# Performance work log

Hardware: AMD Instinct MI355X
Metric: run time of the kernel (lower is better)

## Reference

```python
import jax, jax.numpy as jnp
import numpy as np

# Model constants (from TinyRecursiveModel defaults)
IN = 200        # input feature dim (hard-coded Linear(200, d_model))
D = 64          # d_model
NH = 2          # nhead (head_dim = 32); with seq_len=1 attention is trivial
FF = 64         # dim_feedforward
LAYERS = 2      # TransformerEncoder num_layers
STEPS = 16      # recursion_steps
B = 65536       # batch size
EPS = 1e-5      # torch LayerNorm eps


def setup_inputs() -> dict:
    key = jax.random.key(0)
    ks = jax.random.split(key, 14)
    w = lambda k, shape, s=0.05: (jax.random.normal(k, shape, jnp.float32) * s)
    return {
        "x": jax.random.normal(ks[0], (B, IN), jnp.float32),
        # input_proj: Linear(200, 64)
        "input_w": w(ks[1], (D, IN)), "input_b": w(ks[2], (D,)),
        # per-layer MHA: packed in_proj (q,k,v) and out_proj, stacked over LAYERS
        "Wqkv": w(ks[3], (LAYERS, 3 * D, D)), "bqkv": w(ks[4], (LAYERS, 3 * D)),
        "Wo": w(ks[5], (LAYERS, D, D)), "bo": w(ks[6], (LAYERS, D)),
        "ln1_g": jnp.ones((LAYERS, D), jnp.float32), "ln1_b": jnp.zeros((LAYERS, D), jnp.float32),
        # per-layer FFN: Linear(64,64) -> relu -> Linear(64,64)
        "W1": w(ks[7], (LAYERS, FF, D)), "b1": w(ks[8], (LAYERS, FF)),
        "W2": w(ks[9], (LAYERS, D, FF)), "b2": w(ks[10], (LAYERS, D)),
        "ln2_g": jnp.ones((LAYERS, D), jnp.float32), "ln2_b": jnp.zeros((LAYERS, D), jnp.float32),
        # output_proj: Linear(64, 1)
        "out_w": w(ks[11], (1, D)), "out_b": w(ks[12], (1,)),
    }


def _ln(x, g, b):
    m = jnp.mean(x, axis=-1, keepdims=True)
    v = jnp.var(x, axis=-1, keepdims=True)
    return (x - m) * jax.lax.rsqrt(v + EPS) * g + b


def reference(x, input_w, input_b, Wqkv, bqkv, Wo, bo, ln1_g, ln1_b,
              W1, b1, W2, b2, ln2_g, ln2_b, out_w, out_b):
    h = x @ input_w.T + input_b  # [B, D]; seq dim of size 1 is kept implicit

    def layer(h, l):
        # seq_len == 1: softmax over a single key is identically 1, so the
        # attention output equals V exactly (Q/K have zero influence & zero grad).
        Wv = Wqkv[l, 2 * D:3 * D]
        bv = bqkv[l, 2 * D:3 * D]
        v = h @ Wv.T + bv                     # [B, D]
        sa = v @ Wo[l].T + bo[l]              # out_proj
        h = _ln(h + sa, ln1_g[l], ln1_b[l])   # post-norm (torch default)
        ff = jax.nn.relu(h @ W1[l].T + b1[l]) @ W2[l].T + b2[l]
        return _ln(h + ff, ln2_g[l], ln2_b[l])

    def step(h, _):
        for l in range(LAYERS):  # 2 structurally distinct layers
            h = layer(h, l)
        return h, None

    h, _ = jax.lax.scan(step, h, None, length=STEPS)
    out = h @ out_w.T + out_b  # [B, 1]
    return out[:, 0]           # squeeze -> [B]
```

## Files before the change

kernel.cpp:

```cpp
#include <hip/hip_runtime.h>


using f16x8 = __attribute__((ext_vector_type(8))) _Float16;
using f32x4 = __attribute__((ext_vector_type(4))) float;

#define DI __device__ __forceinline__

namespace {

constexpr int RS = 144;
constexpr float EPS = 1e-5f;

DI unsigned packh2(float a, float b) {
  _Float16 lo = (_Float16)a, hi = (_Float16)b;
  unsigned short ul = __builtin_bit_cast(unsigned short, lo);
  unsigned short uh = __builtin_bit_cast(unsigned short, hi);
  return ((unsigned)uh << 16) | (unsigned)ul;
}

DI f16x8 cvt8h(f32x4 a, f32x4 b) {
  f16x8 r;
  r[0] = (_Float16)a[0]; r[1] = (_Float16)a[1];
  r[2] = (_Float16)a[2]; r[3] = (_Float16)a[3];
  r[4] = (_Float16)b[0]; r[5] = (_Float16)b[1];
  r[6] = (_Float16)b[2]; r[7] = (_Float16)b[3];
  return r;
}

DI unsigned pkmax0(unsigned t) {
  unsigned r;
  asm("v_pk_max_f16 %0, %1, 0" : "=v"(r) : "v"(t));
  return r;
}

DI void swap16(unsigned& a, unsigned& b) {
#if __has_builtin(__builtin_amdgcn_permlane16_swap)
  auto r = __builtin_amdgcn_permlane16_swap(a, b, false, false);
  a = r[0]; b = r[1];
#else
  unsigned ax = (unsigned)__shfl_xor((int)a, 16);
  unsigned bx = (unsigned)__shfl_xor((int)b, 16);
  bool odd = (threadIdx.x & 16) != 0;
  unsigned na = odd ? bx : a;
  unsigned nb = odd ? b : ax;
  a = na; b = nb;
#endif
}
DI void swap32(unsigned& a, unsigned& b) {
#if __has_builtin(__builtin_amdgcn_permlane32_swap)
  auto r = __builtin_amdgcn_permlane32_swap(a, b, false, false);
  a = r[0]; b = r[1];
#else
  unsigned ax = (unsigned)__shfl_xor((int)a, 32);
  unsigned bx = (unsigned)__shfl_xor((int)b, 32);
  bool hi = (threadIdx.x & 32) != 0;
  unsigned na = hi ? bx : a;
  unsigned nb = hi ? b : ax;
  a = na; b = nb;
#endif
}

DI float reduce4(float x) {
  unsigned a = __builtin_bit_cast(unsigned, x), b = a;
  swap16(a, b);
  float x1 = __builtin_bit_cast(float, a) + __builtin_bit_cast(float, b);
  unsigned c = __builtin_bit_cast(unsigned, x1), d = c;
  swap32(c, d);
  return __builtin_bit_cast(float, c) + __builtin_bit_cast(float, d);
}

union BU {
  unsigned u[8];
  struct { f16x8 b0, b1; } f;
};

template <bool RELU>
DI void packacc(const f32x4 (&acc)[4], BU& o) {
#pragma unroll
  for (int tp = 0; tp < 4; ++tp) {
    unsigned p0 = packh2(acc[tp][0], acc[tp][1]);
    unsigned p1 = packh2(acc[tp][2], acc[tp][3]);
    if (RELU) { p0 = pkmax0(p0); p1 = pkmax0(p1); }
    o.u[2 * tp + 0] = p0;
    o.u[2 * tp + 1] = p1;
  }
}

DI void exchange(BU& o) {
  swap32(o.u[0], o.u[2]); swap32(o.u[1], o.u[3]);
  swap32(o.u[4], o.u[6]); swap32(o.u[5], o.u[7]);
  swap16(o.u[0], o.u[2]); swap16(o.u[1], o.u[3]);
  swap16(o.u[4], o.u[6]); swap16(o.u[5], o.u[7]);
}

struct WFrag { f16x8 f[4][2]; };

DI WFrag loadW(const float* W, int l15, int g) {
  WFrag w;
#pragma unroll
  for (int tp = 0; tp < 4; ++tp)
#pragma unroll
    for (int s = 0; s < 2; ++s) {
      const float* p = W + (16 * tp + l15) * 64 + 32 * s + 8 * g;
      w.f[tp][s] = cvt8h(*(const f32x4*)p, *(const f32x4*)(p + 4));
    }
  return w;
}

DI f32x4 mfma(f16x8 a, f16x8 b, f32x4 c) {
  return __builtin_amdgcn_mfma_f32_16x16x32_f16(a, b, c, 0, 0, 0);
}

DI void lnorm(const f32x4 (&a)[4], const float* gb, int g, f32x4 (&h)[4]) {
  float s = 0.f, q = 0.f;
#pragma unroll
  for (int tp = 0; tp < 4; ++tp)
#pragma unroll
    for (int r = 0; r < 4; ++r) { float x = a[tp][r]; s += x; q = fmaf(x, x, q); }
  s = reduce4(s); q = reduce4(q);
  float mean = s * 0.015625f;
  float var  = fmaf(q, 0.015625f, -mean * mean);
  float rs   = rsqrtf(var + EPS);
  float u    = -mean * rs;
  const f32x4* gv = (const f32x4*)gb;
#pragma unroll
  for (int tp = 0; tp < 4; ++tp) {
    f32x4 gg = gv[4 * tp + g];
    f32x4 bb = gv[16 + 4 * tp + g];
#pragma unroll
    for (int r = 0; r < 4; ++r)
      h[tp][r] = fmaf(fmaf(a[tp][r], rs, u), gg[r], bb[r]);
  }
}

struct alignas(16) Smem {
  char  mats[4][64 * RS];
  float params[2 * 7 * 64];
};

DI void do_layer(f32x4 (&h)[4], BU& b, const WFrag& wvo, const char* w1b,
                 const char* w2b, const float* prm, int g) {
  const f32x4* pv = (const f32x4*)prm;
  f32x4 a[4];
#pragma unroll
  for (int tp = 0; tp < 4; ++tp) {
    a[tp] = mfma(wvo.f[tp][1], b.f.b1, mfma(wvo.f[tp][0], b.f.b0, h[tp]));
    a[tp] += pv[4 * tp + g];
  }
  lnorm(a, prm + 192, g, h);
  packacc<false>(h, b);
  exchange(b);
#pragma unroll
  for (int tp = 0; tp < 4; ++tp) {
    f16x8 a0 = *(const f16x8*)(w1b + tp * 16 * RS);
    f16x8 a1 = *(const f16x8*)(w1b + tp * 16 * RS + 64);
    a[tp] = mfma(a1, b.f.b1, mfma(a0, b.f.b0, pv[16 + 4 * tp + g]));
  }
  packacc<true>(a, b);
  exchange(b);
#pragma unroll
  for (int tp = 0; tp < 4; ++tp) {
    f16x8 a0 = *(const f16x8*)(w2b + tp * 16 * RS);
    f16x8 a1 = *(const f16x8*)(w2b + tp * 16 * RS + 64);
    a[tp] = mfma(a1, b.f.b1, mfma(a0, b.f.b0, h[tp]));
    a[tp] += pv[32 + 4 * tp + g];
  }
  lnorm(a, prm + 320, g, h);
  packacc<false>(h, b);
  exchange(b);
}

__global__ __launch_bounds__(256) void precompute_kernel(
    const float* __restrict__ Wqkv, const float* __restrict__ bqkv,
    const float* __restrict__ Wo, const float* __restrict__ bo,
    float* __restrict__ ws) {
  __shared__ float wv[4096];
  __shared__ float wo[4096];
  const int l = blockIdx.x;
  const float* Wv  = Wqkv + l * (192 * 64) + 128 * 64;
  const float* WoL = Wo + l * 4096;
  for (int e = threadIdx.x; e < 4096; e += 256) { wv[e] = Wv[e]; wo[e] = WoL[e]; }
  __syncthreads();
  float* wvo = ws + l * 4096;
  const int i = threadIdx.x >> 2, j0 = (threadIdx.x & 3) * 16;
  float acc[16];
#pragma unroll
  for (int jj = 0; jj < 16; ++jj) acc[jj] = 0.f;
  for (int k = 0; k < 64; ++k) {
    float a = wo[i * 64 + k];
#pragma unroll
    for (int jj = 0; jj < 16; ++jj) acc[jj] = fmaf(a, wv[k * 64 + j0 + jj], acc[jj]);
  }
#pragma unroll
  for (int jj = 0; jj < 16; ++jj) wvo[i * 64 + j0 + jj] = acc[jj];
  if (threadIdx.x < 64) {
    const int i2 = threadIdx.x;
    const float* bv = bqkv + l * 192 + 128;
    float s = bo[l * 64 + i2];
    for (int k = 0; k < 64; ++k) s = fmaf(wo[i2 * 64 + k], bv[k], s);
    ws[2 * 4096 + l * 64 + i2] = s;
  }
}

__global__ __launch_bounds__(256, 2) void trm7_kernel(
    const float* __restrict__ x, const float* __restrict__ input_w,
    const float* __restrict__ input_b, const float* __restrict__ W1,
    const float* __restrict__ b1, const float* __restrict__ W2,
    const float* __restrict__ b2, const float* __restrict__ ln1_g,
    const float* __restrict__ ln1_b, const float* __restrict__ ln2_g,
    const float* __restrict__ ln2_b, const float* __restrict__ out_w,
    const float* __restrict__ out_b, const float* __restrict__ ws,
    float* __restrict__ out) {
  __shared__ Smem sm;
  const int tid = threadIdx.x;
  const int w = tid >> 6, lane = tid & 63;
  const int l15 = lane & 15, g = lane >> 4;
  const int row0 = blockIdx.x * 64 + w * 16;

  {
    const float* srcs[4] = {W1, W1 + 4096, W2, W2 + 4096};
#pragma unroll
    for (int m = 0; m < 4; ++m) {
      char* dst = sm.mats[m];
      const float* src = srcs[m];
      for (int e = tid; e < 512; e += 256) {
        int row = e >> 3, c8 = (e & 7) * 8;
        const float* p = src + row * 64 + c8;
        *(f16x8*)(dst + row * RS + 2 * c8) =
            cvt8h(*(const f32x4*)p, *(const f32x4*)(p + 4));
      }
    }
  }
  for (int e = tid; e < 896; e += 256) {
    int l = e / 448, r = e % 448, v = r >> 6, j = r & 63;
    const float* src;
    switch (v) {
      case 0:  src = ws + 2 * 4096 + l * 64; break;
      case 1:  src = b1 + l * 64; break;
      case 2:  src = b2 + l * 64; break;
      case 3:  src = ln1_g + l * 64; break;
      case 4:  src = ln1_b + l * 64; break;
      case 5:  src = ln2_g + l * 64; break;
      default: src = ln2_b + l * 64; break;
    }
    sm.params[l * 448 + v * 64 + j] = src[j];
  }

  WFrag wvo0 = loadW(ws, l15, g);
  WFrag wvo1 = loadW(ws + 4096, l15, g);

  const char* w1b0 = sm.mats[0] + l15 * RS + 16 * g;
  const char* w1b1 = sm.mats[1] + l15 * RS + 16 * g;
  const char* w2b0 = sm.mats[2] + l15 * RS + 16 * g;
  const char* w2b1 = sm.mats[3] + l15 * RS + 16 * g;

  f32x4 h[4];
#pragma unroll
  for (int tp = 0; tp < 4; ++tp)
    h[tp] = *(const f32x4*)(input_b + 16 * tp + 4 * g);
  {
    const float* xr = x + (size_t)(row0 + l15) * 200;
    const f32x4 zero = {0.f, 0.f, 0.f, 0.f};
    for (int s7 = 0; s7 < 7; ++s7) {
      int kb = 32 * s7 + 8 * g;
      bool v0 = kb < 200;
      f32x4 xa0 = v0 ? *(const f32x4*)(xr + kb) : zero;
      f32x4 xa1 = v0 ? *(const f32x4*)(xr + kb + 4) : zero;
      f16x8 bf = cvt8h(xa0, xa1);
#pragma unroll
      for (int tp = 0; tp < 4; ++tp) {
        const float* wr = input_w + (16 * tp + l15) * 200;
        f32x4 wa = v0 ? *(const f32x4*)(wr + kb) : zero;
        f32x4 wb = v0 ? *(const f32x4*)(wr + kb + 4) : zero;
        h[tp] = mfma(cvt8h(wa, wb), bf, h[tp]);
      }
    }
  }
  BU b;
  packacc<false>(h, b);
  exchange(b);
  __syncthreads();

#pragma unroll 1
  for (int step = 0; step < 16; ++step) {
    do_layer(h, b, wvo0, w1b0, w2b0, sm.params,       g);
    do_layer(h, b, wvo1, w1b1, w2b1, sm.params + 448, g);
  }

  float p = 0.f;
#pragma unroll
  for (int tp = 0; tp < 4; ++tp) {
    f32x4 ow = *(const f32x4*)(out_w + 16 * tp + 4 * g);
#pragma unroll
    for (int r = 0; r < 4; ++r) p = fmaf(h[tp][r], ow[r], p);
  }
  p += __shfl_xor(p, 16);
  p += __shfl_xor(p, 32);
  if (lane < 16) out[row0 + l15] = p + out_b[0];
}

}

extern "C" void kernel_launch(void* const* d_in, const int* in_sizes, int n_in,
                              void* d_out, int out_size, void* d_ws, size_t ws_size,
                              hipStream_t stream) {
  const float* x       = (const float*)d_in[0];
  const float* input_w = (const float*)d_in[1];
  const float* input_b = (const float*)d_in[2];
  const float* Wqkv    = (const float*)d_in[3];
  const float* bqkv    = (const float*)d_in[4];
  const float* Wo      = (const float*)d_in[5];
  const float* bo      = (const float*)d_in[6];
  const float* ln1_g   = (const float*)d_in[7];
  const float* ln1_b   = (const float*)d_in[8];
  const float* W1      = (const float*)d_in[9];
  const float* b1      = (const float*)d_in[10];
  const float* W2      = (const float*)d_in[11];
  const float* b2      = (const float*)d_in[12];
  const float* ln2_g   = (const float*)d_in[13];
  const float* ln2_b   = (const float*)d_in[14];
  const float* out_w   = (const float*)d_in[15];
  const float* out_b   = (const float*)d_in[16];
  float* out = (float*)d_out;
  float* ws  = (float*)d_ws;

  hipLaunchKernelGGL(precompute_kernel, dim3(2), dim3(256), 0, stream,
                     Wqkv, bqkv, Wo, bo, ws);
  hipLaunchKernelGGL(trm7_kernel, dim3(1024), dim3(256), 0, stream,
                     x, input_w, input_b, W1, b1, W2, b2, ln1_g, ln1_b,
                     ln2_g, ln2_b, out_w, out_b, ws, out);
}
```

Before: 127.2 us.

## Permute K layout of weight fragments to drop register exchange shuffles

Reorders the K-dimension packing of the W_vo, W1 and W2 fragments (columns 4g and 4g+16 instead of 8g..8g+7) so that accumulator output packed to fp16 can be fed directly as the next MFMA B operand. This removes the per-matmul cross-lane exchange (swap32/swap16 permutes). It also switches the fp32→fp16 packing to v_cvt_pkrtz, which rounds toward zero instead of to nearest. Finally it moves the bias and LayerNorm parameter gather into the precompute kernel, which writes them to the global workspace, and the main kernel now reads them from global/cache instead of LDS. The rounding mode change slightly alters numerics, and global parameter loads could add latency inside the hot loop.

```diff
diff --git a/kernel.cpp b/kernel.cpp
--- a/kernel.cpp
+++ b/kernel.cpp
@@ -11,11 +11,14 @@
 constexpr int RS = 144;
 constexpr float EPS = 1e-5f;
 
-DI unsigned packh2(float a, float b) {
-  _Float16 lo = (_Float16)a, hi = (_Float16)b;
-  unsigned short ul = __builtin_bit_cast(unsigned short, lo);
-  unsigned short uh = __builtin_bit_cast(unsigned short, hi);
-  return ((unsigned)uh << 16) | (unsigned)ul;
+DI unsigned pkrtz(float a, float b) {
+#if __has_builtin(__builtin_amdgcn_cvt_pkrtz)
+  return __builtin_bit_cast(unsigned, __builtin_amdgcn_cvt_pkrtz(a, b));
+#else
+  unsigned r;
+  asm("v_cvt_pkrtz_f16_f32 %0, %1, %2" : "=v"(r) : "v"(a), "v"(b));
+  return r;
+#endif
 }
 
 DI f16x8 cvt8h(f32x4 a, f32x4 b) {
@@ -78,21 +81,14 @@
 DI void packacc(const f32x4 (&acc)[4], BU& o) {
 #pragma unroll
   for (int tp = 0; tp < 4; ++tp) {
-    unsigned p0 = packh2(acc[tp][0], acc[tp][1]);
-    unsigned p1 = packh2(acc[tp][2], acc[tp][3]);
+    unsigned p0 = pkrtz(acc[tp][0], acc[tp][1]);
+    unsigned p1 = pkrtz(acc[tp][2], acc[tp][3]);
     if (RELU) { p0 = pkmax0(p0); p1 = pkmax0(p1); }
     o.u[2 * tp + 0] = p0;
     o.u[2 * tp + 1] = p1;
   }
 }
 
-DI void exchange(BU& o) {
-  swap32(o.u[0], o.u[2]); swap32(o.u[1], o.u[3]);
-  swap32(o.u[4], o.u[6]); swap32(o.u[5], o.u[7]);
-  swap16(o.u[0], o.u[2]); swap16(o.u[1], o.u[3]);
-  swap16(o.u[4], o.u[6]); swap16(o.u[5], o.u[7]);
-}
-
 struct WFrag { f16x8 f[4][2]; };
 
 DI WFrag loadW(const float* W, int l15, int g) {
@@ -101,8 +97,8 @@
   for (int tp = 0; tp < 4; ++tp)
 #pragma unroll
     for (int s = 0; s < 2; ++s) {
-      const float* p = W + (16 * tp + l15) * 64 + 32 * s + 8 * g;
-      w.f[tp][s] = cvt8h(*(const f32x4*)p, *(const f32x4*)(p + 4));
+      const float* p = W + (16 * tp + l15) * 64 + 32 * s + 4 * g;
+      w.f[tp][s] = cvt8h(*(const f32x4*)p, *(const f32x4*)(p + 16));
     }
   return w;
 }
@@ -134,12 +130,12 @@
 }
 
 struct alignas(16) Smem {
-  char  mats[4][64 * RS];
-  float params[2 * 7 * 64];
+  char mats[4][64 * RS];
 };
 
 DI void do_layer(f32x4 (&h)[4], BU& b, const WFrag& wvo, const char* w1b,
                  const char* w2b, const float* prm, int g) {
+  asm("" : "+r"(prm));
   const f32x4* pv = (const f32x4*)prm;
   f32x4 a[4];
 #pragma unroll
@@ -149,7 +145,6 @@
   }
   lnorm(a, prm + 192, g, h);
   packacc<false>(h, b);
-  exchange(b);
 #pragma unroll
   for (int tp = 0; tp < 4; ++tp) {
     f16x8 a0 = *(const f16x8*)(w1b + tp * 16 * RS);
@@ -157,7 +152,6 @@
     a[tp] = mfma(a1, b.f.b1, mfma(a0, b.f.b0, pv[16 + 4 * tp + g]));
   }
   packacc<true>(a, b);
-  exchange(b);
 #pragma unroll
   for (int tp = 0; tp < 4; ++tp) {
     f16x8 a0 = *(const f16x8*)(w2b + tp * 16 * RS);
@@ -167,12 +161,14 @@
   }
   lnorm(a, prm + 320, g, h);
   packacc<false>(h, b);
-  exchange(b);
 }
 
 __global__ __launch_bounds__(256) void precompute_kernel(
     const float* __restrict__ Wqkv, const float* __restrict__ bqkv,
     const float* __restrict__ Wo, const float* __restrict__ bo,
+    const float* __restrict__ b1, const float* __restrict__ b2,
+    const float* __restrict__ ln1_g, const float* __restrict__ ln1_b,
+    const float* __restrict__ ln2_g, const float* __restrict__ ln2_b,
     float* __restrict__ ws) {
   __shared__ float wv[4096];
   __shared__ float wo[4096];
@@ -193,22 +189,26 @@
   }
 #pragma unroll
   for (int jj = 0; jj < 16; ++jj) wvo[i * 64 + j0 + jj] = acc[jj];
+  float* prm = ws + 2 * 4096 + l * 448;
   if (threadIdx.x < 64) {
     const int i2 = threadIdx.x;
     const float* bv = bqkv + l * 192 + 128;
     float s = bo[l * 64 + i2];
     for (int k = 0; k < 64; ++k) s = fmaf(wo[i2 * 64 + k], bv[k], s);
-    ws[2 * 4096 + l * 64 + i2] = s;
-  }
-}
-
-__global__ __launch_bounds__(256, 2) void trm7_kernel(
+    prm[i2]       = s;
+    prm[64 + i2]  = b1[l * 64 + i2];
+    prm[128 + i2] = b2[l * 64 + i2];
+    prm[192 + i2] = ln1_g[l * 64 + i2];
+    prm[256 + i2] = ln1_b[l * 64 + i2];
+    prm[320 + i2] = ln2_g[l * 64 + i2];
+    prm[384 + i2] = ln2_b[l * 64 + i2];
+  }
+}
+
+__global__ __launch_bounds__(256, 2) void trm9_kernel(
     const float* __restrict__ x, const float* __restrict__ input_w,
     const float* __restrict__ input_b, const float* __restrict__ W1,
-    const float* __restrict__ b1, const float* __restrict__ W2,
-    const float* __restrict__ b2, const float* __restrict__ ln1_g,
-    const float* __restrict__ ln1_b, const float* __restrict__ ln2_g,
-    const float* __restrict__ ln2_b, const float* __restrict__ out_w,
+    const float* __restrict__ W2, const float* __restrict__ out_w,
     const float* __restrict__ out_b, const float* __restrict__ ws,
     float* __restrict__ out) {
   __shared__ Smem sm;
@@ -224,26 +224,12 @@
       char* dst = sm.mats[m];
       const float* src = srcs[m];
       for (int e = tid; e < 512; e += 256) {
-        int row = e >> 3, c8 = (e & 7) * 8;
-        const float* p = src + row * 64 + c8;
-        *(f16x8*)(dst + row * RS + 2 * c8) =
-            cvt8h(*(const f32x4*)p, *(const f32x4*)(p + 4));
+        int row = e >> 3, q = e & 7, s = q >> 2, gq = q & 3;
+        const float* p = src + row * 64 + 32 * s + 4 * gq;
+        *(f16x8*)(dst + row * RS + 64 * s + 16 * gq) =
+            cvt8h(*(const f32x4*)p, *(const f32x4*)(p + 16));
       }
     }
-  }
-  for (int e = tid; e < 896; e += 256) {
-    int l = e / 448, r = e % 448, v = r >> 6, j = r & 63;
-    const float* src;
-    switch (v) {
-      case 0:  src = ws + 2 * 4096 + l * 64; break;
-      case 1:  src = b1 + l * 64; break;
-      case 2:  src = b2 + l * 64; break;
-      case 3:  src = ln1_g + l * 64; break;
-      case 4:  src = ln1_b + l * 64; break;
-      case 5:  src = ln2_g + l * 64; break;
-      default: src = ln2_b + l * 64; break;
-    }
-    sm.params[l * 448 + v * 64 + j] = src[j];
   }
 
   WFrag wvo0 = loadW(ws, l15, g);
@@ -253,6 +239,8 @@
   const char* w1b1 = sm.mats[1] + l15 * RS + 16 * g;
   const char* w2b0 = sm.mats[2] + l15 * RS + 16 * g;
   const char* w2b1 = sm.mats[3] + l15 * RS + 16 * g;
+  const float* prm0 = ws + 2 * 4096;
+  const float* prm1 = ws + 2 * 4096 + 448;
 
   f32x4 h[4];
 #pragma unroll
@@ -278,13 +266,12 @@
   }
   BU b;
   packacc<false>(h, b);
-  exchange(b);
   __syncthreads();
 
 #pragma unroll 1
   for (int step = 0; step < 16; ++step) {
-    do_layer(h, b, wvo0, w1b0, w2b0, sm.params,       g);
-    do_layer(h, b, wvo1, w1b1, w2b1, sm.params + 448, g);
+    do_layer(h, b, wvo0, w1b0, w2b0, prm0, g);
+    do_layer(h, b, wvo1, w1b1, w2b1, prm1, g);
   }
 
   float p = 0.f;
@@ -325,8 +312,7 @@
   float* ws  = (float*)d_ws;
 
   hipLaunchKernelGGL(precompute_kernel, dim3(2), dim3(256), 0, stream,
-                     Wqkv, bqkv, Wo, bo, ws);
-  hipLaunchKernelGGL(trm7_kernel, dim3(1024), dim3(256), 0, stream,
-                     x, input_w, input_b, W1, b1, W2, b2, ln1_g, ln1_b,
-                     ln2_g, ln2_b, out_w, out_b, ws, out);
-}
+                     Wqkv, bqkv, Wo, bo, b1, b2, ln1_g, ln1_b, ln2_g, ln2_b, ws);
+  hipLaunchKernelGGL(trm9_kernel, dim3(1024), dim3(256), 0, stream,
+                     x, input_w, input_b, W1, W2, out_w, out_b, ws, out);
+}
```

New measurement: 176.9 us. +39.1%, slower.
